# Kernel optimization log

Measured on AMD Instinct MI355X. Metric: run time of the kernel, lower is better.

## Reference

```python
import jax, jax.numpy as jnp
import numpy as np

B, S, DIM = 64, 576, 768
KEEP_TOKEN = 64  # module keeps KEEP_TOKEN-1 top patches + 1 pooled extra token
HID = 128       # autoencoder bottleneck


def setup_inputs() -> dict:
    key = jax.random.key(0)
    k1, k2, k3, k4 = jax.random.split(key, 4)
    cls_emb = jax.random.normal(k1, (B, DIM), dtype=jnp.float32)
    fm = jax.random.normal(k2, (B, S, DIM), dtype=jnp.float32)
    # autoencoder: Linear(dim,128) -> Tanh -> Linear(128,dim); y = x @ W + b
    W1 = jax.random.normal(k3, (DIM, HID), dtype=jnp.float32) / np.sqrt(DIM)
    b1 = jnp.zeros((HID,), dtype=jnp.float32)
    W2 = jax.random.normal(k4, (HID, DIM), dtype=jnp.float32) / np.sqrt(HID)
    b2 = jnp.zeros((DIM,), dtype=jnp.float32)
    return {"cls_emb": cls_emb, "fm": fm, "W1": W1, "b1": b1, "W2": W2, "b2": b2}


def reference(cls_emb, fm, W1, b1, W2, b2):
    # cls attention scores over patch tokens: [B, S]
    cls_attn = jnp.einsum('bd,bsd->bs', cls_emb, fm)
    # top-(K-1) patches by cls attention (largest, sorted)
    _, idx = jax.lax.top_k(cls_attn, KEEP_TOKEN - 1)           # [B, K-1]
    top_token = jnp.take_along_axis(fm, idx[:, :, None], axis=1)  # [B, K-1, DIM]
    # mask selected positions (one_hot(idx).sum(1) -> 0/1 since topk idx unique)
    batch_ix = jnp.arange(fm.shape[0])[:, None]
    one_hot_idx = jnp.zeros_like(cls_attn).at[batch_ix, idx].add(1.0)  # [B, S]
    weight = jax.nn.softmax(one_hot_idx * -10000.0 + cls_attn, axis=1)[:, :, None]
    extra_token = jnp.sum(weight * fm, axis=1, keepdims=True)  # [B, 1, DIM]
    visual_tokens = jnp.concatenate([top_token, extra_token], axis=1)  # [B, K, DIM]
    ae = lambda x: jnp.tanh(x @ W1 + b1) @ W2 + b2
    return ae(visual_tokens), ae(cls_emb)
```

## Files before the change

### kernel.cpp

```cpp
#include <hip/hip_runtime.h>
#include <math.h>

#define BB   64
#define SS   576
#define DD   768
#define KTOP 63
#define KEEP 64
#define HH   128
#define NROW (BB*KEEP + BB)
#define SCH  24

typedef unsigned long long ull;
typedef _Float16 h2 __attribute__((ext_vector_type(2)));

static __device__ __forceinline__ float DOT2(h2 a, h2 b, float c) {
#if __has_builtin(__builtin_amdgcn_fdot2)
  return __builtin_amdgcn_fdot2(a, b, c, false);
#else
  return fmaf((float)a[1], (float)b[1], fmaf((float)a[0], (float)b[0], c));
#endif
}
static __device__ __forceinline__ unsigned PK(float x, float y) {
  return __builtin_bit_cast(unsigned, __builtin_amdgcn_cvt_pkrtz(x, y));
}
static __device__ __forceinline__ h2 BC(unsigned u) {
  return __builtin_bit_cast(h2, u);
}

__global__ __launch_bounds__(256) void k_scores(const float* __restrict__ cls,
                                                const float* __restrict__ fm,
                                                float* __restrict__ scores)
{
  int gw = (blockIdx.x * blockDim.x + threadIdx.x) >> 6;
  int lane = threadIdx.x & 63;
  if (gw >= BB * SS) return;
  int b = gw / SS, s = gw - b * SS;
  const float4* frow = (const float4*)(fm + ((size_t)b * SS + s) * DD);
  const float4* crow = (const float4*)(cls + (size_t)b * DD);
  double acc = 0.0;
#pragma unroll
  for (int j = 0; j < 3; ++j) {
    float4 f = frow[lane + 64 * j];
    float4 c = crow[lane + 64 * j];
    acc += (double)f.x * c.x + (double)f.y * c.y + (double)f.z * c.z + (double)f.w * c.w;
  }
#pragma unroll
  for (int off = 32; off > 0; off >>= 1) acc += __shfl_down(acc, off, 64);
  if (lane == 0) scores[(size_t)b * SS + s] = (float)acc;
}

__global__ __launch_bounds__(576) void k_rank(const float* __restrict__ scores,
                                              int* __restrict__ idxout,
                                              float* __restrict__ wprime)
{
  __shared__ ull keys[SS];
  __shared__ float redm[9], redz[9];
  int b = blockIdx.x, tid = threadIdx.x;
  int lane = tid & 63, wid = tid >> 6;
  float sc = scores[(size_t)b * SS + tid];
  unsigned int u = __float_as_uint(sc);
  u = (u & 0x80000000u) ? ~u : (u | 0x80000000u);
  ull key = ((ull)u << 32) | (ull)(0xFFFFFFFFu - (unsigned)tid);
  keys[tid] = key;
  __syncthreads();
  int rank = 0;
#pragma unroll 8
  for (int s = 0; s < SS; ++s) rank += (keys[s] > key) ? 1 : 0;
  bool sel = rank < KTOP;
  if (sel) idxout[b * KEEP + rank] = tid;
  float m = sel ? -1e30f : sc;
#pragma unroll
  for (int off = 32; off; off >>= 1) m = fmaxf(m, __shfl_xor(m, off, 64));
  if (lane == 0) redm[wid] = m;
  __syncthreads();
  float M = redm[0];
#pragma unroll
  for (int i = 1; i < 9; ++i) M = fmaxf(M, redm[i]);
  float e = sel ? 0.f : expf(sc - M);
  float z = e;
#pragma unroll
  for (int off = 32; off; off >>= 1) z += __shfl_xor(z, off, 64);
  if (lane == 0) redz[wid] = z;
  __syncthreads();
  float Z = redz[0];
#pragma unroll
  for (int i = 1; i < 9; ++i) Z += redz[i];
  wprime[(size_t)b * SS + tid] = e / Z;
}

__global__ __launch_bounds__(192) void k_extra2(const float* __restrict__ wprime,
                                                const float* __restrict__ fm,
                                                float* __restrict__ epart)
{
  int b = blockIdx.x, p = blockIdx.y, tid = threadIdx.x;
  const float* fbase = fm + ((size_t)b * SS + p * SCH) * DD + tid * 4;
  const float* wp = wprime + (size_t)b * SS + p * SCH;
  float4 acc = make_float4(0.f, 0.f, 0.f, 0.f);
#pragma unroll
  for (int r = 0; r < SCH; ++r) {
    float w = wp[r];
    float4 v = *(const float4*)(fbase + (size_t)r * DD);
    acc.x = fmaf(w, v.x, acc.x); acc.y = fmaf(w, v.y, acc.y);
    acc.z = fmaf(w, v.z, acc.z); acc.w = fmaf(w, v.w, acc.w);
  }
  *(float4*)(epart + ((size_t)(b * SCH + p) * DD) + tid * 4) = acc;
}

__global__ __launch_bounds__(256) void k_ered(const float* __restrict__ epart,
                                              float* __restrict__ extra)
{
  int i = blockIdx.x * 256 + threadIdx.x;
  int b = i / (DD / 4), c4 = i - b * (DD / 4);
  const float4* P = (const float4*)epart;
  float4 s = make_float4(0.f, 0.f, 0.f, 0.f);
#pragma unroll
  for (int p = 0; p < SCH; ++p) {
    float4 t = P[(size_t)(b * SCH + p) * (DD / 4) + c4];
    s.x += t.x; s.y += t.y; s.z += t.z; s.w += t.w;
  }
  ((float4*)extra)[i] = s;
}

template<int CPB>
__global__ __launch_bounds__(128) void k_ae1(const float* __restrict__ fm,
                                             const float* __restrict__ cls,
                                             const float* __restrict__ extra,
                                             const int* __restrict__ idxin,
                                             const float* __restrict__ W1,
                                             float* __restrict__ partial)
{
  __shared__ _Float16 Xs[64][68];
  __shared__ unsigned Wp[32][132];
  __shared__ const float* rowptr[64];
  int g = blockIdx.x;
  int tid = threadIdx.x;

  if (tid < 64) {
    const float* p;
    if (g < BB) {
      p = (tid < KTOP) ? fm + ((size_t)g * SS + idxin[g * KEEP + tid]) * DD
                       : extra + (size_t)g * DD;
    } else {
      p = cls + (size_t)tid * DD;
    }
    rowptr[tid] = p;
  }

  int ty = tid >> 4, tx = tid & 15;
  int r0 = ty * 8;
  float acc[8][8] = {};

  for (int cc = 0; cc < CPB; ++cc) {
    int kb = (blockIdx.y * CPB + cc) * 64;
    __syncthreads();
#pragma unroll
    for (int i = 0; i < 8; ++i) {
      int id = tid + 128 * i;
      int k4 = id & 15, r = id >> 4;
      float4 v = *(const float4*)(rowptr[r] + kb + k4 * 4);
      uint2 o = { PK(v.x, v.y), PK(v.z, v.w) };
      *(uint2*)&Xs[r][k4 * 4] = o;
    }
#pragma unroll
    for (int i = 0; i < 8; ++i) {
      int id = tid + 128 * i;
      int c4 = id & 31, kp = id >> 5;
      const float* w0 = W1 + (size_t)(kb + 2 * kp) * HH + c4 * 4;
      float4 a = *(const float4*)w0;
      float4 b = *(const float4*)(w0 + HH);
      uint4 o = { PK(a.x, b.x), PK(a.y, b.y), PK(a.z, b.z), PK(a.w, b.w) };
      *(uint4*)&Wp[kp][c4 * 4] = o;
    }
    __syncthreads();
#pragma unroll 4
    for (int q = 0; q < 16; ++q) {
      uint2 xr[8];
#pragma unroll
      for (int i = 0; i < 8; ++i) xr[i] = *(const uint2*)&Xs[r0 + i][q * 4];
      uint4 wa0 = *(const uint4*)&Wp[2 * q][tx * 4];
      uint4 wa1 = *(const uint4*)&Wp[2 * q][64 + tx * 4];
      uint4 wb0 = *(const uint4*)&Wp[2 * q + 1][tx * 4];
      uint4 wb1 = *(const uint4*)&Wp[2 * q + 1][64 + tx * 4];
#pragma unroll
      for (int i = 0; i < 8; ++i) {
        h2 a0 = BC(xr[i].x), a1 = BC(xr[i].y);
        acc[i][0] = DOT2(a1, BC(wb0.x), DOT2(a0, BC(wa0.x), acc[i][0]));
        acc[i][1] = DOT2(a1, BC(wb0.y), DOT2(a0, BC(wa0.y), acc[i][1]));
        acc[i][2] = DOT2(a1, BC(wb0.z), DOT2(a0, BC(wa0.z), acc[i][2]));
        acc[i][3] = DOT2(a1, BC(wb0.w), DOT2(a0, BC(wa0.w), acc[i][3]));
        acc[i][4] = DOT2(a1, BC(wb1.x), DOT2(a0, BC(wa1.x), acc[i][4]));
        acc[i][5] = DOT2(a1, BC(wb1.y), DOT2(a0, BC(wa1.y), acc[i][5]));
        acc[i][6] = DOT2(a1, BC(wb1.z), DOT2(a0, BC(wa1.z), acc[i][6]));
        acc[i][7] = DOT2(a1, BC(wb1.w), DOT2(a0, BC(wa1.w), acc[i][7]));
      }
    }
  }
  float* P = partial + (size_t)(CPB == 1 ? blockIdx.y : 0) * ((size_t)NROW * HH);
#pragma unroll
  for (int i = 0; i < 8; ++i) {
    size_t row = (size_t)(g * 64 + r0 + i);
    float4 v0 = make_float4(acc[i][0], acc[i][1], acc[i][2], acc[i][3]);
    float4 v1 = make_float4(acc[i][4], acc[i][5], acc[i][6], acc[i][7]);
    *(float4*)&P[row * HH + tx * 4] = v0;
    *(float4*)&P[row * HH + 64 + tx * 4] = v1;
  }
}

template<int NP>
__global__ __launch_bounds__(256) void k_hred(const float* __restrict__ partial,
                                              const float* __restrict__ b1,
                                              unsigned* __restrict__ H16)
{
  int i4 = blockIdx.x * 256 + threadIdx.x;
  const float4* P = (const float4*)partial;
  float4 s = P[i4];
#pragma unroll
  for (int p = 1; p < NP; ++p) {
    float4 t = P[(size_t)p * (NROW * HH / 4) + i4];
    s.x += t.x; s.y += t.y; s.z += t.z; s.w += t.w;
  }
  float4 bv = ((const float4*)b1)[i4 & 31];
  s.x = tanhf(s.x + bv.x); s.y = tanhf(s.y + bv.y);
  s.z = tanhf(s.z + bv.z); s.w = tanhf(s.w + bv.w);
  uint2 o = { PK(s.x, s.y), PK(s.z, s.w) };
  ((uint2*)H16)[i4] = o;
}

__global__ __launch_bounds__(128) void k_ae2(const unsigned* __restrict__ H16,
                                             const float* __restrict__ W2,
                                             const float* __restrict__ b2,
                                             float* __restrict__ out)
{
  __shared__ _Float16 Hs[64][132];
  __shared__ unsigned Wp[64][132];
  int g = blockIdx.x, cb = blockIdx.y, tid = threadIdx.x;

#pragma unroll
  for (int i = 0; i < 16; ++i) {
    int id = tid + 128 * i;
    int k4 = id & 31, r = id >> 5;
    uint2 v = ((const uint2*)H16)[(size_t)(g * 64 + r) * (HH / 4) + k4];
    *(uint2*)&Hs[r][k4 * 4] = v;
  }
#pragma unroll
  for (int i = 0; i < 16; ++i) {
    int id = tid + 128 * i;
    int c4 = id & 31, kp = id >> 5;
    const float* w0 = W2 + (size_t)(2 * kp) * DD + cb * 128 + c4 * 4;
    float4 a = *(const float4*)w0;
    float4 b = *(const float4*)(w0 + DD);
    uint4 o = { PK(a.x, b.x), PK(a.y, b.y), PK(a.z, b.z), PK(a.w, b.w) };
    *(uint4*)&Wp[kp][c4 * 4] = o;
  }
  __syncthreads();

  int ty = tid >> 4, tx = tid & 15;
  int r0 = ty * 8;
  float acc[8][8] = {};
#pragma unroll 4
  for (int q = 0; q < 32; ++q) {
    uint2 xr[8];
#pragma unroll
    for (int i = 0; i < 8; ++i) xr[i] = *(const uint2*)&Hs[r0 + i][q * 4];
    uint4 wa0 = *(const uint4*)&Wp[2 * q][tx * 4];
    uint4 wa1 = *(const uint4*)&Wp[2 * q][64 + tx * 4];
    uint4 wb0 = *(const uint4*)&Wp[2 * q + 1][tx * 4];
    uint4 wb1 = *(const uint4*)&Wp[2 * q + 1][64 + tx * 4];
#pragma unroll
    for (int i = 0; i < 8; ++i) {
      h2 a0 = BC(xr[i].x), a1 = BC(xr[i].y);
      acc[i][0] = DOT2(a1, BC(wb0.x), DOT2(a0, BC(wa0.x), acc[i][0]));
      acc[i][1] = DOT2(a1, BC(wb0.y), DOT2(a0, BC(wa0.y), acc[i][1]));
      acc[i][2] = DOT2(a1, BC(wb0.z), DOT2(a0, BC(wa0.z), acc[i][2]));
      acc[i][3] = DOT2(a1, BC(wb0.w), DOT2(a0, BC(wa0.w), acc[i][3]));
      acc[i][4] = DOT2(a1, BC(wb1.x), DOT2(a0, BC(wa1.x), acc[i][4]));
      acc[i][5] = DOT2(a1, BC(wb1.y), DOT2(a0, BC(wa1.y), acc[i][5]));
      acc[i][6] = DOT2(a1, BC(wb1.z), DOT2(a0, BC(wa1.z), acc[i][6]));
      acc[i][7] = DOT2(a1, BC(wb1.w), DOT2(a0, BC(wa1.w), acc[i][7]));
    }
  }
  float4 bv0 = *(const float4*)&b2[cb * 128 + tx * 4];
  float4 bv1 = *(const float4*)&b2[cb * 128 + 64 + tx * 4];
#pragma unroll
  for (int i = 0; i < 8; ++i) {
    size_t row = (size_t)(g * 64 + r0 + i);
    float4 y0 = make_float4(acc[i][0] + bv0.x, acc[i][1] + bv0.y,
                            acc[i][2] + bv0.z, acc[i][3] + bv0.w);
    float4 y1 = make_float4(acc[i][4] + bv1.x, acc[i][5] + bv1.y,
                            acc[i][6] + bv1.z, acc[i][7] + bv1.w);
    *(float4*)&out[row * DD + cb * 128 + tx * 4] = y0;
    *(float4*)&out[row * DD + cb * 128 + 64 + tx * 4] = y1;
  }
}

extern "C" void kernel_launch(void* const* d_in, const int* in_sizes, int n_in,
                              void* d_out, int out_size, void* d_ws, size_t ws_size,
                              hipStream_t stream)
{
  const float* cls = (const float*)d_in[0];
  const float* fm  = (const float*)d_in[1];
  const float* W1  = (const float*)d_in[2];
  const float* b1  = (const float*)d_in[3];
  const float* W2  = (const float*)d_in[4];
  const float* b2  = (const float*)d_in[5];
  float* out = (float*)d_out;

  char* ws = (char*)d_ws;
  float* scores  = (float*)ws;
  int*   idx     = (int*)(ws + 147456);
  float* extra   = (float*)(ws + 163840);
  float* wprime  = (float*)(ws + 360448);
  float* epart   = (float*)(ws + 507904);
  float* partial = (float*)(ws + 5226496);
  const size_t PSLICE = (size_t)NROW * HH * 4;
  const size_t H16SZ  = (size_t)NROW * HH * 2;

  hipLaunchKernelGGL(k_scores, dim3((BB * SS) / 4), dim3(256), 0, stream, cls, fm, scores);
  hipLaunchKernelGGL(k_rank,   dim3(BB),            dim3(576), 0, stream, scores, idx, wprime);
  hipLaunchKernelGGL(k_extra2, dim3(BB, SCH),       dim3(192), 0, stream, wprime, fm, epart);
  hipLaunchKernelGGL(k_ered,   dim3(BB * DD / 1024), dim3(256), 0, stream, epart, extra);

  if (ws_size >= 5226496 + 12 * PSLICE + H16SZ) {
    unsigned* H16 = (unsigned*)(ws + 5226496 + 12 * PSLICE);
    hipLaunchKernelGGL(k_ae1<1>,  dim3(65, 12),      dim3(128), 0, stream,
                       fm, cls, extra, idx, W1, partial);
    hipLaunchKernelGGL(k_hred<12>, dim3(NROW * HH / 1024), dim3(256), 0, stream,
                       partial, b1, H16);
    hipLaunchKernelGGL(k_ae2,     dim3(65, 6),       dim3(128), 0, stream, H16, W2, b2, out);
  } else {
    unsigned* H16 = (unsigned*)(ws + 5226496 + PSLICE);
    hipLaunchKernelGGL(k_ae1<12>, dim3(65, 1),       dim3(128), 0, stream,
                       fm, cls, extra, idx, W1, partial);
    hipLaunchKernelGGL(k_hred<1>, dim3(NROW * HH / 1024), dim3(256), 0, stream,
                       partial, b1, H16);
    hipLaunchKernelGGL(k_ae2,     dim3(65, 6),       dim3(128), 0, stream, H16, W2, b2, out);
  }
}
```

Baseline: 100.9 us.

## Fuse all stages into one cooperative persistent kernel with grid syncs

Replaces the seven separate launches (scores, rank, extra partial, extra reduce, AE1, hidden reduce, AE2) with a single cooperative kernel of 256 blocks that steps through the stages, separated by grid.sync(). Each stage is rewritten as a grid-stride loop, the per-block GEMM tiles are retiled for 256 threads (4 rows per thread), and the shared memory for the stages is overlaid in a union. The aim is to remove launch gaps and the tail effect between kernels. In exchange only 256 blocks run, so stages with little parallelism such as the 64-block rank step leave most CUs idle, and each grid barrier has its own cost. The workspace-size fallback path is dropped, so the kernel now always assumes the full 12-slice partial buffer fits.

```diff
diff --git a/kernel.cpp b/kernel.cpp
--- a/kernel.cpp
+++ b/kernel.cpp
@@ -1,5 +1,8 @@
 #include <hip/hip_runtime.h>
+#include <hip/hip_cooperative_groups.h>
 #include <math.h>
+
+namespace cg = cooperative_groups;
 
 #define BB   64
 #define SS   576
@@ -27,269 +30,281 @@
   return __builtin_bit_cast(h2, u);
 }
 
-__global__ __launch_bounds__(256) void k_scores(const float* __restrict__ cls,
-                                                const float* __restrict__ fm,
-                                                float* __restrict__ scores)
+__global__ __launch_bounds__(256, 1) void k_mega(
+    const float* __restrict__ cls, const float* __restrict__ fm,
+    const float* __restrict__ W1, const float* __restrict__ b1,
+    const float* __restrict__ W2, const float* __restrict__ b2,
+    float* __restrict__ out,
+    float* __restrict__ scores, int* __restrict__ idx,
+    float* __restrict__ wprime, float* __restrict__ epart,
+    float* __restrict__ extra, float* __restrict__ partial,
+    unsigned* __restrict__ H16)
 {
-  int gw = (blockIdx.x * blockDim.x + threadIdx.x) >> 6;
-  int lane = threadIdx.x & 63;
-  if (gw >= BB * SS) return;
-  int b = gw / SS, s = gw - b * SS;
-  const float4* frow = (const float4*)(fm + ((size_t)b * SS + s) * DD);
-  const float4* crow = (const float4*)(cls + (size_t)b * DD);
-  double acc = 0.0;
-#pragma unroll
-  for (int j = 0; j < 3; ++j) {
-    float4 f = frow[lane + 64 * j];
-    float4 c = crow[lane + 64 * j];
-    acc += (double)f.x * c.x + (double)f.y * c.y + (double)f.z * c.z + (double)f.w * c.w;
-  }
-#pragma unroll
-  for (int off = 32; off > 0; off >>= 1) acc += __shfl_down(acc, off, 64);
-  if (lane == 0) scores[(size_t)b * SS + s] = (float)acc;
-}
-
-__global__ __launch_bounds__(576) void k_rank(const float* __restrict__ scores,
-                                              int* __restrict__ idxout,
-                                              float* __restrict__ wprime)
-{
-  __shared__ ull keys[SS];
-  __shared__ float redm[9], redz[9];
-  int b = blockIdx.x, tid = threadIdx.x;
-  int lane = tid & 63, wid = tid >> 6;
-  float sc = scores[(size_t)b * SS + tid];
-  unsigned int u = __float_as_uint(sc);
-  u = (u & 0x80000000u) ? ~u : (u | 0x80000000u);
-  ull key = ((ull)u << 32) | (ull)(0xFFFFFFFFu - (unsigned)tid);
-  keys[tid] = key;
-  __syncthreads();
-  int rank = 0;
+  cg::grid_group grid = cg::this_grid();
+  __shared__ union {
+    ull keys[SS];
+    struct { _Float16 Xs[64][68]; unsigned Wp[32][132]; } a1;
+    struct { _Float16 Hs[64][132]; unsigned Wp[64][132]; } a2;
+  } sh;
+  __shared__ const float* rowptr[64];
+  __shared__ float redA[4], redB[4];
+
+  const int tid = threadIdx.x;
+  const int B = blockIdx.x;
+  const int lane = tid & 63, wid = tid >> 6;
+
+  {
+    int wv = (B << 2) + wid;
+#pragma unroll 2
+    for (int k = 0; k < 36; k += 2) {
+      int rowA = wv + (k << 10), rowB = rowA + 1024;
+      int bA = rowA / SS, sA = rowA - bA * SS;
+      int bB = rowB / SS, sB = rowB - bB * SS;
+      const float4* fA = (const float4*)(fm + ((size_t)bA * SS + sA) * DD);
+      const float4* cA = (const float4*)(cls + (size_t)bA * DD);
+      const float4* fB = (const float4*)(fm + ((size_t)bB * SS + sB) * DD);
+      const float4* cB = (const float4*)(cls + (size_t)bB * DD);
+      double aA = 0.0, aB = 0.0;
+#pragma unroll
+      for (int j = 0; j < 3; ++j) {
+        float4 f1 = fA[lane + 64 * j], c1 = cA[lane + 64 * j];
+        float4 f2 = fB[lane + 64 * j], c2 = cB[lane + 64 * j];
+        aA += (double)f1.x*c1.x + (double)f1.y*c1.y + (double)f1.z*c1.z + (double)f1.w*c1.w;
+        aB += (double)f2.x*c2.x + (double)f2.y*c2.y + (double)f2.z*c2.z + (double)f2.w*c2.w;
+      }
+#pragma unroll
+      for (int off = 32; off > 0; off >>= 1) {
+        aA += __shfl_down(aA, off, 64);
+        aB += __shfl_down(aB, off, 64);
+      }
+      if (lane == 0) { scores[rowA] = (float)aA; scores[rowB] = (float)aB; }
+    }
+  }
+  grid.sync();
+
+  if (B < BB) {
+    int b = B;
+    for (int s = tid; s < SS; s += 256) {
+      unsigned u = __float_as_uint(scores[(size_t)b * SS + s]);
+      u = (u & 0x80000000u) ? ~u : (u | 0x80000000u);
+      sh.keys[s] = ((ull)u << 32) | (ull)(0xFFFFFFFFu - (unsigned)s);
+    }
+    __syncthreads();
+    int s0 = tid, s1 = tid + 256, s2 = tid + 512;
+    bool h3 = (s2 < SS);
+    ull k0 = sh.keys[s0], k1 = sh.keys[s1], k2 = h3 ? sh.keys[s2] : 0ull;
+    int r0 = 0, r1 = 0, r2 = 0;
 #pragma unroll 8
-  for (int s = 0; s < SS; ++s) rank += (keys[s] > key) ? 1 : 0;
-  bool sel = rank < KTOP;
-  if (sel) idxout[b * KEEP + rank] = tid;
-  float m = sel ? -1e30f : sc;
-#pragma unroll
-  for (int off = 32; off; off >>= 1) m = fmaxf(m, __shfl_xor(m, off, 64));
-  if (lane == 0) redm[wid] = m;
-  __syncthreads();
-  float M = redm[0];
-#pragma unroll
-  for (int i = 1; i < 9; ++i) M = fmaxf(M, redm[i]);
-  float e = sel ? 0.f : expf(sc - M);
-  float z = e;
-#pragma unroll
-  for (int off = 32; off; off >>= 1) z += __shfl_xor(z, off, 64);
-  if (lane == 0) redz[wid] = z;
-  __syncthreads();
-  float Z = redz[0];
-#pragma unroll
-  for (int i = 1; i < 9; ++i) Z += redz[i];
-  wprime[(size_t)b * SS + tid] = e / Z;
-}
-
-__global__ __launch_bounds__(192) void k_extra2(const float* __restrict__ wprime,
-                                                const float* __restrict__ fm,
-                                                float* __restrict__ epart)
-{
-  int b = blockIdx.x, p = blockIdx.y, tid = threadIdx.x;
-  const float* fbase = fm + ((size_t)b * SS + p * SCH) * DD + tid * 4;
-  const float* wp = wprime + (size_t)b * SS + p * SCH;
-  float4 acc = make_float4(0.f, 0.f, 0.f, 0.f);
-#pragma unroll
-  for (int r = 0; r < SCH; ++r) {
-    float w = wp[r];
-    float4 v = *(const float4*)(fbase + (size_t)r * DD);
-    acc.x = fmaf(w, v.x, acc.x); acc.y = fmaf(w, v.y, acc.y);
-    acc.z = fmaf(w, v.z, acc.z); acc.w = fmaf(w, v.w, acc.w);
-  }
-  *(float4*)(epart + ((size_t)(b * SCH + p) * DD) + tid * 4) = acc;
-}
-
-__global__ __launch_bounds__(256) void k_ered(const float* __restrict__ epart,
-                                              float* __restrict__ extra)
-{
-  int i = blockIdx.x * 256 + threadIdx.x;
-  int b = i / (DD / 4), c4 = i - b * (DD / 4);
-  const float4* P = (const float4*)epart;
-  float4 s = make_float4(0.f, 0.f, 0.f, 0.f);
-#pragma unroll
-  for (int p = 0; p < SCH; ++p) {
-    float4 t = P[(size_t)(b * SCH + p) * (DD / 4) + c4];
-    s.x += t.x; s.y += t.y; s.z += t.z; s.w += t.w;
-  }
-  ((float4*)extra)[i] = s;
-}
-
-template<int CPB>
-__global__ __launch_bounds__(128) void k_ae1(const float* __restrict__ fm,
-                                             const float* __restrict__ cls,
-                                             const float* __restrict__ extra,
-                                             const int* __restrict__ idxin,
-                                             const float* __restrict__ W1,
-                                             float* __restrict__ partial)
-{
-  __shared__ _Float16 Xs[64][68];
-  __shared__ unsigned Wp[32][132];
-  __shared__ const float* rowptr[64];
-  int g = blockIdx.x;
-  int tid = threadIdx.x;
-
-  if (tid < 64) {
-    const float* p;
-    if (g < BB) {
-      p = (tid < KTOP) ? fm + ((size_t)g * SS + idxin[g * KEEP + tid]) * DD
-                       : extra + (size_t)g * DD;
-    } else {
-      p = cls + (size_t)tid * DD;
-    }
-    rowptr[tid] = p;
-  }
-
-  int ty = tid >> 4, tx = tid & 15;
-  int r0 = ty * 8;
-  float acc[8][8] = {};
-
-  for (int cc = 0; cc < CPB; ++cc) {
-    int kb = (blockIdx.y * CPB + cc) * 64;
-    __syncthreads();
-#pragma unroll
-    for (int i = 0; i < 8; ++i) {
-      int id = tid + 128 * i;
+    for (int i = 0; i < SS; ++i) {
+      ull kk = sh.keys[i];
+      r0 += kk > k0; r1 += kk > k1; r2 += kk > k2;
+    }
+    float sc0 = scores[(size_t)b * SS + s0];
+    float sc1 = scores[(size_t)b * SS + s1];
+    float sc2 = h3 ? scores[(size_t)b * SS + s2] : -1e30f;
+    bool sel0 = r0 < KTOP, sel1 = r1 < KTOP, sel2 = h3 && (r2 < KTOP);
+    if (sel0) idx[b * KEEP + r0] = s0;
+    if (sel1) idx[b * KEEP + r1] = s1;
+    if (sel2) idx[b * KEEP + r2] = s2;
+    float m = sel0 ? -1e30f : sc0;
+    if (!sel1) m = fmaxf(m, sc1);
+    if (h3 && !sel2) m = fmaxf(m, sc2);
+#pragma unroll
+    for (int off = 32; off; off >>= 1) m = fmaxf(m, __shfl_xor(m, off, 64));
+    if (lane == 0) redA[wid] = m;
+    __syncthreads();
+    float M = fmaxf(fmaxf(redA[0], redA[1]), fmaxf(redA[2], redA[3]));
+    float e0 = sel0 ? 0.f : expf(sc0 - M);
+    float e1 = sel1 ? 0.f : expf(sc1 - M);
+    float e2 = (h3 && !sel2) ? expf(sc2 - M) : 0.f;
+    float z = e0 + e1 + e2;
+#pragma unroll
+    for (int off = 32; off; off >>= 1) z += __shfl_xor(z, off, 64);
+    if (lane == 0) redB[wid] = z;
+    __syncthreads();
+    float Z = (redB[0] + redB[1]) + (redB[2] + redB[3]);
+    wprime[(size_t)b * SS + s0] = e0 / Z;
+    wprime[(size_t)b * SS + s1] = e1 / Z;
+    if (h3) wprime[(size_t)b * SS + s2] = e2 / Z;
+  }
+  grid.sync();
+
+  for (int t = B; t < BB * SCH; t += 256) {
+    int b = t / SCH, p = t - b * SCH;
+    if (tid < 192) {
+      const float* fbase = fm + ((size_t)b * SS + p * SCH) * DD + tid * 4;
+      const float* wp = wprime + (size_t)b * SS + p * SCH;
+      float4 acc = make_float4(0.f, 0.f, 0.f, 0.f);
+#pragma unroll
+      for (int r = 0; r < SCH; ++r) {
+        float w = wp[r];
+        float4 v = *(const float4*)(fbase + (size_t)r * DD);
+        acc.x = fmaf(w, v.x, acc.x); acc.y = fmaf(w, v.y, acc.y);
+        acc.z = fmaf(w, v.z, acc.z); acc.w = fmaf(w, v.w, acc.w);
+      }
+      *(float4*)(epart + (size_t)(b * SCH + p) * DD + tid * 4) = acc;
+    }
+  }
+  grid.sync();
+
+  {
+    int i = B * 256 + tid;
+    if (i < BB * DD / 4) {
+      int b = i / (DD / 4), c4 = i - b * (DD / 4);
+      const float4* P = (const float4*)epart;
+      float4 s = make_float4(0.f, 0.f, 0.f, 0.f);
+#pragma unroll
+      for (int p = 0; p < SCH; ++p) {
+        float4 t4 = P[(size_t)(b * SCH + p) * (DD / 4) + c4];
+        s.x += t4.x; s.y += t4.y; s.z += t4.z; s.w += t4.w;
+      }
+      ((float4*)extra)[i] = s;
+    }
+  }
+  grid.sync();
+
+  for (int t = B; t < 65 * 12; t += 256) {
+    int g = t % 65, y = t / 65;
+    __syncthreads();
+    if (tid < 64) {
+      const float* p;
+      if (g < BB) p = (tid < KTOP) ? fm + ((size_t)g * SS + idx[g * KEEP + tid]) * DD
+                                   : extra + (size_t)g * DD;
+      else        p = cls + (size_t)tid * DD;
+      rowptr[tid] = p;
+    }
+    __syncthreads();
+    int kb = y * 64;
+#pragma unroll
+    for (int i = 0; i < 4; ++i) {
+      int id = tid + 256 * i;
       int k4 = id & 15, r = id >> 4;
       float4 v = *(const float4*)(rowptr[r] + kb + k4 * 4);
       uint2 o = { PK(v.x, v.y), PK(v.z, v.w) };
-      *(uint2*)&Xs[r][k4 * 4] = o;
-    }
-#pragma unroll
-    for (int i = 0; i < 8; ++i) {
-      int id = tid + 128 * i;
+      *(uint2*)&sh.a1.Xs[r][k4 * 4] = o;
+    }
+#pragma unroll
+    for (int i = 0; i < 4; ++i) {
+      int id = tid + 256 * i;
       int c4 = id & 31, kp = id >> 5;
       const float* w0 = W1 + (size_t)(kb + 2 * kp) * HH + c4 * 4;
       float4 a = *(const float4*)w0;
-      float4 b = *(const float4*)(w0 + HH);
-      uint4 o = { PK(a.x, b.x), PK(a.y, b.y), PK(a.z, b.z), PK(a.w, b.w) };
-      *(uint4*)&Wp[kp][c4 * 4] = o;
-    }
-    __syncthreads();
+      float4 bq = *(const float4*)(w0 + HH);
+      uint4 o = { PK(a.x, bq.x), PK(a.y, bq.y), PK(a.z, bq.z), PK(a.w, bq.w) };
+      *(uint4*)&sh.a1.Wp[kp][c4 * 4] = o;
+    }
+    __syncthreads();
+    int ty = tid >> 4, tx = tid & 15;
+    int rr0 = ty * 4;
+    float acc[4][8] = {};
 #pragma unroll 4
     for (int q = 0; q < 16; ++q) {
-      uint2 xr[8];
-#pragma unroll
-      for (int i = 0; i < 8; ++i) xr[i] = *(const uint2*)&Xs[r0 + i][q * 4];
-      uint4 wa0 = *(const uint4*)&Wp[2 * q][tx * 4];
-      uint4 wa1 = *(const uint4*)&Wp[2 * q][64 + tx * 4];
-      uint4 wb0 = *(const uint4*)&Wp[2 * q + 1][tx * 4];
-      uint4 wb1 = *(const uint4*)&Wp[2 * q + 1][64 + tx * 4];
-#pragma unroll
-      for (int i = 0; i < 8; ++i) {
-        h2 a0 = BC(xr[i].x), a1 = BC(xr[i].y);
-        acc[i][0] = DOT2(a1, BC(wb0.x), DOT2(a0, BC(wa0.x), acc[i][0]));
-        acc[i][1] = DOT2(a1, BC(wb0.y), DOT2(a0, BC(wa0.y), acc[i][1]));
-        acc[i][2] = DOT2(a1, BC(wb0.z), DOT2(a0, BC(wa0.z), acc[i][2]));
-        acc[i][3] = DOT2(a1, BC(wb0.w), DOT2(a0, BC(wa0.w), acc[i][3]));
-        acc[i][4] = DOT2(a1, BC(wb1.x), DOT2(a0, BC(wa1.x), acc[i][4]));
-        acc[i][5] = DOT2(a1, BC(wb1.y), DOT2(a0, BC(wa1.y), acc[i][5]));
-        acc[i][6] = DOT2(a1, BC(wb1.z), DOT2(a0, BC(wa1.z), acc[i][6]));
-        acc[i][7] = DOT2(a1, BC(wb1.w), DOT2(a0, BC(wa1.w), acc[i][7]));
-      }
-    }
-  }
-  float* P = partial + (size_t)(CPB == 1 ? blockIdx.y : 0) * ((size_t)NROW * HH);
-#pragma unroll
-  for (int i = 0; i < 8; ++i) {
-    size_t row = (size_t)(g * 64 + r0 + i);
-    float4 v0 = make_float4(acc[i][0], acc[i][1], acc[i][2], acc[i][3]);
-    float4 v1 = make_float4(acc[i][4], acc[i][5], acc[i][6], acc[i][7]);
-    *(float4*)&P[row * HH + tx * 4] = v0;
-    *(float4*)&P[row * HH + 64 + tx * 4] = v1;
-  }
-}
-
-template<int NP>
-__global__ __launch_bounds__(256) void k_hred(const float* __restrict__ partial,
-                                              const float* __restrict__ b1,
-                                              unsigned* __restrict__ H16)
-{
-  int i4 = blockIdx.x * 256 + threadIdx.x;
-  const float4* P = (const float4*)partial;
-  float4 s = P[i4];
-#pragma unroll
-  for (int p = 1; p < NP; ++p) {
-    float4 t = P[(size_t)p * (NROW * HH / 4) + i4];
-    s.x += t.x; s.y += t.y; s.z += t.z; s.w += t.w;
-  }
-  float4 bv = ((const float4*)b1)[i4 & 31];
-  s.x = tanhf(s.x + bv.x); s.y = tanhf(s.y + bv.y);
-  s.z = tanhf(s.z + bv.z); s.w = tanhf(s.w + bv.w);
-  uint2 o = { PK(s.x, s.y), PK(s.z, s.w) };
-  ((uint2*)H16)[i4] = o;
-}
-
-__global__ __launch_bounds__(128) void k_ae2(const unsigned* __restrict__ H16,
-                                             const float* __restrict__ W2,
-                                             const float* __restrict__ b2,
-                                             float* __restrict__ out)
-{
-  __shared__ _Float16 Hs[64][132];
-  __shared__ unsigned Wp[64][132];
-  int g = blockIdx.x, cb = blockIdx.y, tid = threadIdx.x;
-
-#pragma unroll
-  for (int i = 0; i < 16; ++i) {
-    int id = tid + 128 * i;
-    int k4 = id & 31, r = id >> 5;
-    uint2 v = ((const uint2*)H16)[(size_t)(g * 64 + r) * (HH / 4) + k4];
-    *(uint2*)&Hs[r][k4 * 4] = v;
-  }
-#pragma unroll
-  for (int i = 0; i < 16; ++i) {
-    int id = tid + 128 * i;
-    int c4 = id & 31, kp = id >> 5;
-    const float* w0 = W2 + (size_t)(2 * kp) * DD + cb * 128 + c4 * 4;
-    float4 a = *(const float4*)w0;
-    float4 b = *(const float4*)(w0 + DD);
-    uint4 o = { PK(a.x, b.x), PK(a.y, b.y), PK(a.z, b.z), PK(a.w, b.w) };
-    *(uint4*)&Wp[kp][c4 * 4] = o;
-  }
-  __syncthreads();
-
-  int ty = tid >> 4, tx = tid & 15;
-  int r0 = ty * 8;
-  float acc[8][8] = {};
+      uint2 xr[4];
+#pragma unroll
+      for (int i = 0; i < 4; ++i) xr[i] = *(const uint2*)&sh.a1.Xs[rr0 + i][q * 4];
+      uint4 wa0 = *(const uint4*)&sh.a1.Wp[2 * q][tx * 4];
+      uint4 wa1 = *(const uint4*)&sh.a1.Wp[2 * q][64 + tx * 4];
+      uint4 wb0 = *(const uint4*)&sh.a1.Wp[2 * q + 1][tx * 4];
+      uint4 wb1 = *(const uint4*)&sh.a1.Wp[2 * q + 1][64 + tx * 4];
+#pragma unroll
+      for (int i = 0; i < 4; ++i) {
+        h2 a0 = BC(xr[i].x), a1v = BC(xr[i].y);
+        acc[i][0] = DOT2(a1v, BC(wb0.x), DOT2(a0, BC(wa0.x), acc[i][0]));
+        acc[i][1] = DOT2(a1v, BC(wb0.y), DOT2(a0, BC(wa0.y), acc[i][1]));
+        acc[i][2] = DOT2(a1v, BC(wb0.z), DOT2(a0, BC(wa0.z), acc[i][2]));
+        acc[i][3] = DOT2(a1v, BC(wb0.w), DOT2(a0, BC(wa0.w), acc[i][3]));
+        acc[i][4] = DOT2(a1v, BC(wb1.x), DOT2(a0, BC(wa1.x), acc[i][4]));
+        acc[i][5] = DOT2(a1v, BC(wb1.y), DOT2(a0, BC(wa1.y), acc[i][5]));
+        acc[i][6] = DOT2(a1v, BC(wb1.z), DOT2(a0, BC(wa1.z), acc[i][6]));
+        acc[i][7] = DOT2(a1v, BC(wb1.w), DOT2(a0, BC(wa1.w), acc[i][7]));
+      }
+    }
+    float* P = partial + (size_t)y * ((size_t)NROW * HH);
+#pragma unroll
+    for (int i = 0; i < 4; ++i) {
+      size_t row = (size_t)(g * 64 + rr0 + i);
+      float4 v0 = make_float4(acc[i][0], acc[i][1], acc[i][2], acc[i][3]);
+      float4 v1 = make_float4(acc[i][4], acc[i][5], acc[i][6], acc[i][7]);
+      *(float4*)&P[row * HH + tx * 4] = v0;
+      *(float4*)&P[row * HH + 64 + tx * 4] = v1;
+    }
+  }
+  grid.sync();
+
+  for (int i4 = B * 256 + tid; i4 < NROW * HH / 4; i4 += 65536) {
+    const float4* P = (const float4*)partial;
+    float4 s = P[i4];
+#pragma unroll
+    for (int p = 1; p < 12; ++p) {
+      float4 t4 = P[(size_t)p * (NROW * HH / 4) + i4];
+      s.x += t4.x; s.y += t4.y; s.z += t4.z; s.w += t4.w;
+    }
+    float4 bv = ((const float4*)b1)[i4 & 31];
+    s.x = tanhf(s.x + bv.x); s.y = tanhf(s.y + bv.y);
+    s.z = tanhf(s.z + bv.z); s.w = tanhf(s.w + bv.w);
+    uint2 o = { PK(s.x, s.y), PK(s.z, s.w) };
+    ((uint2*)H16)[i4] = o;
+  }
+  grid.sync();
+
+  for (int t = B; t < 65 * 6; t += 256) {
+    int g = t % 65, cb = t / 65;
+    __syncthreads();
+#pragma unroll
+    for (int i = 0; i < 8; ++i) {
+      int id = tid + 256 * i;
+      int k4 = id & 31, r = id >> 5;
+      uint2 v = ((const uint2*)H16)[(size_t)(g * 64 + r) * (HH / 4) + k4];
+      *(uint2*)&sh.a2.Hs[r][k4 * 4] = v;
+    }
+#pragma unroll
+    for (int i = 0; i < 8; ++i) {
+      int id = tid + 256 * i;
+      int c4 = id & 31, kp = id >> 5;
+      const float* w0 = W2 + (size_t)(2 * kp) * DD + cb * 128 + c4 * 4;
+      float4 a = *(const float4*)w0;
+      float4 bq = *(const float4*)(w0 + DD);
+      uint4 o = { PK(a.x, bq.x), PK(a.y, bq.y), PK(a.z, bq.z), PK(a.w, bq.w) };
+      *(uint4*)&sh.a2.Wp[kp][c4 * 4] = o;
+    }
+    __syncthreads();
+    int ty = tid >> 4, tx = tid & 15;
+    int rr0 = ty * 4;
+    float acc[4][8] = {};
 #pragma unroll 4
-  for (int q = 0; q < 32; ++q) {
-    uint2 xr[8];
-#pragma unroll
-    for (int i = 0; i < 8; ++i) xr[i] = *(const uint2*)&Hs[r0 + i][q * 4];
-    uint4 wa0 = *(const uint4*)&Wp[2 * q][tx * 4];
-    uint4 wa1 = *(const uint4*)&Wp[2 * q][64 + tx * 4];
-    uint4 wb0 = *(const uint4*)&Wp[2 * q + 1][tx * 4];
-    uint4 wb1 = *(const uint4*)&Wp[2 * q + 1][64 + tx * 4];
-#pragma unroll
-    for (int i = 0; i < 8; ++i) {
-      h2 a0 = BC(xr[i].x), a1 = BC(xr[i].y);
-      acc[i][0] = DOT2(a1, BC(wb0.x), DOT2(a0, BC(wa0.x), acc[i][0]));
-      acc[i][1] = DOT2(a1, BC(wb0.y), DOT2(a0, BC(wa0.y), acc[i][1]));
-      acc[i][2] = DOT2(a1, BC(wb0.z), DOT2(a0, BC(wa0.z), acc[i][2]));
-      acc[i][3] = DOT2(a1, BC(wb0.w), DOT2(a0, BC(wa0.w), acc[i][3]));
-      acc[i][4] = DOT2(a1, BC(wb1.x), DOT2(a0, BC(wa1.x), acc[i][4]));
-      acc[i][5] = DOT2(a1, BC(wb1.y), DOT2(a0, BC(wa1.y), acc[i][5]));
-      acc[i][6] = DOT2(a1, BC(wb1.z), DOT2(a0, BC(wa1.z), acc[i][6]));
-      acc[i][7] = DOT2(a1, BC(wb1.w), DOT2(a0, BC(wa1.w), acc[i][7]));
-    }
-  }
-  float4 bv0 = *(const float4*)&b2[cb * 128 + tx * 4];
-  float4 bv1 = *(const float4*)&b2[cb * 128 + 64 + tx * 4];
-#pragma unroll
-  for (int i = 0; i < 8; ++i) {
-    size_t row = (size_t)(g * 64 + r0 + i);
-    float4 y0 = make_float4(acc[i][0] + bv0.x, acc[i][1] + bv0.y,
-                            acc[i][2] + bv0.z, acc[i][3] + bv0.w);
-    float4 y1 = make_float4(acc[i][4] + bv1.x, acc[i][5] + bv1.y,
-                            acc[i][6] + bv1.z, acc[i][7] + bv1.w);
-    *(float4*)&out[row * DD + cb * 128 + tx * 4] = y0;
-    *(float4*)&out[row * DD + cb * 128 + 64 + tx * 4] = y1;
+    for (int q = 0; q < 32; ++q) {
+      uint2 xr[4];
+#pragma unroll
+      for (int i = 0; i < 4; ++i) xr[i] = *(const uint2*)&sh.a2.Hs[rr0 + i][q * 4];
+      uint4 wa0 = *(const uint4*)&sh.a2.Wp[2 * q][tx * 4];
+      uint4 wa1 = *(const uint4*)&sh.a2.Wp[2 * q][64 + tx * 4];
+      uint4 wb0 = *(const uint4*)&sh.a2.Wp[2 * q + 1][tx * 4];
+      uint4 wb1 = *(const uint4*)&sh.a2.Wp[2 * q + 1][64 + tx * 4];
+#pragma unroll
+      for (int i = 0; i < 4; ++i) {
+        h2 a0 = BC(xr[i].x), a1v = BC(xr[i].y);
+        acc[i][0] = DOT2(a1v, BC(wb0.x), DOT2(a0, BC(wa0.x), acc[i][0]));
+        acc[i][1] = DOT2(a1v, BC(wb0.y), DOT2(a0, BC(wa0.y), acc[i][1]));
+        acc[i][2] = DOT2(a1v, BC(wb0.z), DOT2(a0, BC(wa0.z), acc[i][2]));
+        acc[i][3] = DOT2(a1v, BC(wb0.w), DOT2(a0, BC(wa0.w), acc[i][3]));
+        acc[i][4] = DOT2(a1v, BC(wb1.x), DOT2(a0, BC(wa1.x), acc[i][4]));
+        acc[i][5] = DOT2(a1v, BC(wb1.y), DOT2(a0, BC(wa1.y), acc[i][5]));
+        acc[i][6] = DOT2(a1v, BC(wb1.z), DOT2(a0, BC(wa1.z), acc[i][6]));
+        acc[i][7] = DOT2(a1v, BC(wb1.w), DOT2(a0, BC(wa1.w), acc[i][7]));
+      }
+    }
+    float4 bv0 = *(const float4*)&b2[cb * 128 + tx * 4];
+    float4 bv1 = *(const float4*)&b2[cb * 128 + 64 + tx * 4];
+#pragma unroll
+    for (int i = 0; i < 4; ++i) {
+      size_t row = (size_t)(g * 64 + rr0 + i);
+      float4 y0 = make_float4(acc[i][0] + bv0.x, acc[i][1] + bv0.y,
+                              acc[i][2] + bv0.z, acc[i][3] + bv0.w);
+      float4 y1 = make_float4(acc[i][4] + bv1.x, acc[i][5] + bv1.y,
+                              acc[i][6] + bv1.z, acc[i][7] + bv1.w);
+      *(float4*)&out[row * DD + cb * 128 + tx * 4] = y0;
+      *(float4*)&out[row * DD + cb * 128 + 64 + tx * 4] = y1;
+    }
   }
 }
 
@@ -306,33 +321,17 @@
   float* out = (float*)d_out;
 
   char* ws = (char*)d_ws;
-  float* scores  = (float*)ws;
-  int*   idx     = (int*)(ws + 147456);
-  float* extra   = (float*)(ws + 163840);
-  float* wprime  = (float*)(ws + 360448);
-  float* epart   = (float*)(ws + 507904);
-  float* partial = (float*)(ws + 5226496);
-  const size_t PSLICE = (size_t)NROW * HH * 4;
-  const size_t H16SZ  = (size_t)NROW * HH * 2;
-
-  hipLaunchKernelGGL(k_scores, dim3((BB * SS) / 4), dim3(256), 0, stream, cls, fm, scores);
-  hipLaunchKernelGGL(k_rank,   dim3(BB),            dim3(576), 0, stream, scores, idx, wprime);
-  hipLaunchKernelGGL(k_extra2, dim3(BB, SCH),       dim3(192), 0, stream, wprime, fm, epart);
-  hipLaunchKernelGGL(k_ered,   dim3(BB * DD / 1024), dim3(256), 0, stream, epart, extra);
-
-  if (ws_size >= 5226496 + 12 * PSLICE + H16SZ) {
-    unsigned* H16 = (unsigned*)(ws + 5226496 + 12 * PSLICE);
-    hipLaunchKernelGGL(k_ae1<1>,  dim3(65, 12),      dim3(128), 0, stream,
-                       fm, cls, extra, idx, W1, partial);
-    hipLaunchKernelGGL(k_hred<12>, dim3(NROW * HH / 1024), dim3(256), 0, stream,
-                       partial, b1, H16);
-    hipLaunchKernelGGL(k_ae2,     dim3(65, 6),       dim3(128), 0, stream, H16, W2, b2, out);
-  } else {
-    unsigned* H16 = (unsigned*)(ws + 5226496 + PSLICE);
-    hipLaunchKernelGGL(k_ae1<12>, dim3(65, 1),       dim3(128), 0, stream,
-                       fm, cls, extra, idx, W1, partial);
-    hipLaunchKernelGGL(k_hred<1>, dim3(NROW * HH / 1024), dim3(256), 0, stream,
-                       partial, b1, H16);
-    hipLaunchKernelGGL(k_ae2,     dim3(65, 6),       dim3(128), 0, stream, H16, W2, b2, out);
-  }
-}
+  float*    scores  = (float*)ws;
+  int*      idx     = (int*)(ws + 147456);
+  float*    extra   = (float*)(ws + 163840);
+  float*    wprime  = (float*)(ws + 360448);
+  float*    epart   = (float*)(ws + 507904);
+  float*    partial = (float*)(ws + 5226496);
+  unsigned* H16     = (unsigned*)(ws + 5226496 + 12 * 2129920);
+
+  void* args[] = { (void*)&cls, (void*)&fm, (void*)&W1, (void*)&b1,
+                   (void*)&W2, (void*)&b2, (void*)&out,
+                   (void*)&scores, (void*)&idx, (void*)&wprime, (void*)&epart,
+                   (void*)&extra, (void*)&partial, (void*)&H16 };
+  hipLaunchCooperativeKernel((const void*)k_mega, dim3(256), dim3(256), args, 0, stream);
+}
```

Result: slower. 271.7 us (+169.3%).
